# Kernel optimization log

Hardware: AMD Instinct MI355X
Metric: run time of the kernel (lower is better)

The kernel has to match this reference:

```python
import jax, jax.numpy as jnp
import numpy as np

NUM_HEADS = 8
NUM_LEVELS = 4
NUM_POINTS = 4
EMBED_DIM = 256
HEAD_DIM = EMBED_DIM // NUM_HEADS  # 32
SUM_POINTS = NUM_LEVELS * NUM_POINTS  # 16
OFFSET_SCALE = 0.5
SPATIAL = [(80, 80), (40, 40), (20, 20), (10, 10)]


def _bilinear_gather(v_flat, x, y, H, W):
    """grid_sample(bilinear, padding zeros, align_corners=False) via gathers.
    v_flat: (BN, c, H*W); x, y: (BN, Lq, P) pixel coords. -> (BN, c, Lq*P)"""
    BN = v_flat.shape[0]
    x0 = jnp.floor(x)
    y0 = jnp.floor(y)
    wx1 = x - x0
    wy1 = y - y0

    def corner(xi, yi, w):
        valid = (xi >= 0) & (xi <= W - 1) & (yi >= 0) & (yi <= H - 1)
        xc = jnp.clip(xi, 0, W - 1).astype(jnp.int32)
        yc = jnp.clip(yi, 0, H - 1).astype(jnp.int32)
        idx = (yc * W + xc).reshape(BN, -1)  # (BN, Lq*P)
        g = jnp.take_along_axis(v_flat, idx[:, None, :], axis=2)  # (BN, c, Lq*P)
        return g * (w * valid).reshape(BN, 1, -1)

    return (corner(x0, y0, (1.0 - wx1) * (1.0 - wy1))
            + corner(x0 + 1.0, y0, wx1 * (1.0 - wy1))
            + corner(x0, y0 + 1.0, (1.0 - wx1) * wy1)
            + corner(x0 + 1.0, y0 + 1.0, wx1 * wy1))


def setup_inputs() -> dict:
    key = jax.random.key(0)
    ks = jax.random.split(key, 6)
    bs, Lq = 16, 300
    spatial = np.array(SPATIAL, dtype=np.int64)
    Lv = int((spatial[:, 0] * spatial[:, 1]).sum())  # 8500

    query = jax.random.normal(ks[0], (bs, Lq, EMBED_DIM), jnp.float32)
    reference_points = jax.random.uniform(ks[1], (bs, Lq, 1, 4), jnp.float32)  # cx,cy,w,h in (0,1)
    value = jax.random.normal(ks[2], (bs, NUM_HEADS, HEAD_DIM, Lv), jnp.float32)

    W_off = jax.random.normal(ks[3], (EMBED_DIM, NUM_HEADS * SUM_POINTS * 2), jnp.float32) * 0.01
    # bias from _reset_parameters grid init
    thetas = np.arange(NUM_HEADS, dtype=np.float32) * (2.0 * np.pi / NUM_HEADS)
    grid = np.stack([np.cos(thetas), np.sin(thetas)], -1)
    grid = grid / np.abs(grid).max(-1, keepdims=True)
    grid = np.tile(grid.reshape(NUM_HEADS, 1, 2), (1, SUM_POINTS, 1))
    scaling = np.concatenate([np.arange(1, NUM_POINTS + 1) for _ in range(NUM_LEVELS)]).reshape(1, -1, 1)
    b_off = jnp.asarray((grid * scaling).reshape(-1), jnp.float32)

    W_attn = jax.random.normal(ks[4], (EMBED_DIM, NUM_HEADS * SUM_POINTS), jnp.float32) * 0.01
    b_attn = jnp.zeros((NUM_HEADS * SUM_POINTS,), jnp.float32)
    num_points_scale = jnp.full((SUM_POINTS,), 1.0 / NUM_POINTS, jnp.float32)

    return {"query": query, "reference_points": reference_points, "value": value,
            "value_spatial_shapes": spatial, "W_off": W_off, "b_off": b_off,
            "W_attn": W_attn, "b_attn": b_attn, "num_points_scale": num_points_scale}


def reference(query, reference_points, value, value_spatial_shapes,
              W_off, b_off, W_attn, b_attn, num_points_scale):
    bs, Lq, _ = query.shape
    BN = bs * NUM_HEADS

    off = (query @ W_off + b_off).reshape(bs, Lq, NUM_HEADS, SUM_POINTS, 2)
    attn = jax.nn.softmax((query @ W_attn + b_attn).reshape(bs, Lq, NUM_HEADS, SUM_POINTS), axis=-1)

    # box branch: reference_points (bs, Lq, 1, 4); [..., 2:] = wh scales offsets
    offset = off * num_points_scale[:, None] * reference_points[:, :, None, :, 2:] * OFFSET_SCALE
    loc = reference_points[:, :, None, :, :2] + offset  # (bs, Lq, H, SUM_POINTS, 2) in [0,1]

    grids = 2.0 * loc - 1.0
    grids = jnp.transpose(grids, (0, 2, 1, 3, 4)).reshape(BN, Lq, SUM_POINTS, 2)
    attn = jnp.transpose(attn, (0, 2, 1, 3)).reshape(BN, 1, Lq, SUM_POINTS)

    shapes = np.asarray(value_spatial_shapes)
    lvl_sizes = (shapes[:, 0] * shapes[:, 1]).tolist()
    v_levels = jnp.split(value.reshape(BN, HEAD_DIM, -1), np.cumsum(lvl_sizes)[:-1], axis=2)
    g_levels = jnp.split(grids, np.arange(NUM_POINTS, SUM_POINTS, NUM_POINTS), axis=2)

    sampled = []
    for (H, W), v_l, g_l in zip(shapes.tolist(), v_levels, g_levels):
        # align_corners=False pixel coords
        x = (g_l[..., 0] + 1.0) * (W * 0.5) - 0.5
        y = (g_l[..., 1] + 1.0) * (H * 0.5) - 0.5
        s = _bilinear_gather(v_l, x, y, H, W).reshape(BN, HEAD_DIM, Lq, NUM_POINTS)
        sampled.append(s)
    sampled = jnp.concatenate(sampled, axis=-1)  # (BN, c, Lq, SUM_POINTS)

    out = (sampled * attn).sum(-1)  # (BN, c, Lq)
    out = out.reshape(bs, NUM_HEADS * HEAD_DIM, Lq).transpose(0, 2, 1)  # (bs, Lq, embed_dim)
    return out
```

## Files before the change

kernel.cpp:

```cpp
#include <hip/hip_runtime.h>
#include <hip/hip_bf16.h>
#include <hip/hip_fp16.h>
#include <math.h>

#define BS 16
#define LQ 300
#define NH 8
#define HD 32
#define SP 16
#define ED 256
#define LV 8500
#define NB_BLK 300
#define PXT 256
#define TR_PER_BN 34
#define NTR_BLK (TR_PER_BN * 128)

static __device__ __forceinline__ int imin(int a, int b) { return a < b ? a : b; }
static __device__ __forceinline__ int imax(int a, int b) { return a > b ? a : b; }

static __device__ __forceinline__ unsigned f2bf(float x) {
    unsigned u = __float_as_uint(x);
    return (u + 0x7fffu + ((u >> 16) & 1u)) >> 16;
}

static __device__ __forceinline__ unsigned pk2h(float a, float b) {
    __half ha = __float2half_rn(a), hb = __float2half_rn(b);
    unsigned short ua = *reinterpret_cast<unsigned short*>(&ha);
    unsigned short ub = *reinterpret_cast<unsigned short*>(&hb);
    return (unsigned)ua | ((unsigned)ub << 16);
}

static __device__ __forceinline__ float2 up2h(unsigned u) {
    unsigned short ua = (unsigned short)(u & 0xffffu);
    unsigned short ub = (unsigned short)(u >> 16);
    __half ha = *reinterpret_cast<__half*>(&ua);
    __half hb = *reinterpret_cast<__half*>(&ub);
    return make_float2(__half2float(ha), __half2float(hb));
}

static __device__ __forceinline__ void gload16(const float* g, float* l) {
    __builtin_amdgcn_global_load_lds(
        (const __attribute__((address_space(1))) void*)g,
        (__attribute__((address_space(3))) void*)l, 16, 0, 0);
}

__global__ __launch_bounds__(256) void kF(const float* __restrict__ query,
                                          const float* __restrict__ refp,
                                          const float* __restrict__ Woff,
                                          const float* __restrict__ boff,
                                          const float* __restrict__ Wattn,
                                          const float* __restrict__ battn,
                                          const float* __restrict__ nps,
                                          unsigned* __restrict__ la,
                                          const float* __restrict__ v,
                                          __hip_bfloat16* __restrict__ vt,
                                          int nb) {
    __shared__ float s[32 * 256];
    const int tid = threadIdx.x;

    if ((int)blockIdx.x >= nb) {
        const int t   = blockIdx.x - nb;
        const int bn  = t / TR_PER_BN;
        const int px0 = (t - bn * TR_PER_BN) * PXT;
        const int nlv = imin(PXT, LV - px0);

        const int w = tid >> 6;
        const int l = tid & 63;
        if (l * 4 < nlv) {
            const float* src = v + ((size_t)bn * HD + w * 8) * LV + px0 + l * 4;
#pragma unroll
            for (int k = 0; k < 8; ++k)
                gload16(src + (size_t)k * LV, s + (w * 8 + k) * 256);
        }
        __syncthreads();
        const int p2 = tid >> 2;
        const int q  = tid & 3;
        char* dst0 = (char*)vt + ((size_t)bn * LV + px0) * (HD * 2) + q * 16;
#pragma unroll
        for (int j = 0; j < 4; ++j) {
            int p = p2 + 64 * j;
            if (p < nlv) {
                unsigned pk[4];
#pragma unroll
                for (int i = 0; i < 4; ++i) {
                    float f0 = s[(8 * q + 2 * i) * 256 + p];
                    float f1 = s[(8 * q + 2 * i + 1) * 256 + p];
                    pk[i] = f2bf(f0) | (f2bf(f1) << 16);
                }
                *reinterpret_cast<uint4*>(dst0 + (size_t)p * 64) =
                    make_uint4(pk[0], pk[1], pk[2], pk[3]);
            }
        }
        return;
    }

    float* qbuf = s;
    float* lbuf = s;
    const int gq0 = blockIdx.x * 16;

    const float* qsrc = query + (size_t)gq0 * ED;
#pragma unroll
    for (int i = 0; i < 16; ++i) qbuf[tid + 256 * i] = qsrc[tid + 256 * i];
    __syncthreads();

    const int qi = tid >> 5;
    const int cl = tid & 31;
    const float* qa = qbuf + qi * ED;
    const float* qb = qbuf + (qi + 8) * ED;

    float a0[4] = {0,0,0,0}, a1[4] = {0,0,0,0}, a2[4] = {0,0,0,0};
    float c0[4] = {0,0,0,0}, c1[4] = {0,0,0,0}, c2[4] = {0,0,0,0};
    const float4* w0 = (const float4*)(Woff + cl * 4);
    const float4* w1 = (const float4*)(Woff + 128 + cl * 4);
    const float4* w2 = (const float4*)(Wattn + cl * 4);
#pragma unroll 4
    for (int k = 0; k < ED; ++k) {
        float va = qa[k], vb = qb[k];
        float4 x0 = w0[k * 64];
        float4 x1 = w1[k * 64];
        float4 x2 = w2[k * 32];
        a0[0] += va * x0.x; a0[1] += va * x0.y; a0[2] += va * x0.z; a0[3] += va * x0.w;
        a1[0] += va * x1.x; a1[1] += va * x1.y; a1[2] += va * x1.z; a1[3] += va * x1.w;
        a2[0] += va * x2.x; a2[1] += va * x2.y; a2[2] += va * x2.z; a2[3] += va * x2.w;
        c0[0] += vb * x0.x; c0[1] += vb * x0.y; c0[2] += vb * x0.z; c0[3] += vb * x0.w;
        c1[0] += vb * x1.x; c1[1] += vb * x1.y; c1[2] += vb * x1.z; c1[3] += vb * x1.w;
        c2[0] += vb * x2.x; c2[1] += vb * x2.y; c2[2] += vb * x2.z; c2[3] += vb * x2.w;
    }
    __syncthreads();
    {
        float* ra = lbuf + qi * 384;
        float* rb = lbuf + (qi + 8) * 384;
#pragma unroll
        for (int u = 0; u < 4; ++u) {
            float bo0 = boff[cl * 4 + u];
            float bo1 = boff[128 + cl * 4 + u];
            float ba  = battn[cl * 4 + u];
            ra[cl * 4 + u]       = a0[u] + bo0;
            ra[128 + cl * 4 + u] = a1[u] + bo1;
            ra[256 + cl * 4 + u] = a2[u] + ba;
            rb[cl * 4 + u]       = c0[u] + bo0;
            rb[128 + cl * 4 + u] = c1[u] + bo1;
            rb[256 + cl * 4 + u] = c2[u] + ba;
        }
    }
    __syncthreads();

#pragma unroll
    for (int it = 0; it < 2; ++it) {
        const int slot = it * 256 + tid;
        const int qi2 = slot >> 5;
        const int h2  = (slot >> 2) & 7;
        const int pg  = slot & 3;
        const float* lr = lbuf + qi2 * 384;

        float l[4];
#pragma unroll
        for (int i = 0; i < 4; ++i) l[i] = lr[256 + h2 * 16 + pg * 4 + i];
        float m = fmaxf(fmaxf(l[0], l[1]), fmaxf(l[2], l[3]));
        m = fmaxf(m, __shfl_xor(m, 1));
        m = fmaxf(m, __shfl_xor(m, 2));
        float e[4];
        float ps = 0.f;
#pragma unroll
        for (int i = 0; i < 4; ++i) { e[i] = expf(l[i] - m); ps += e[i]; }
        ps += __shfl_xor(ps, 1);
        ps += __shfl_xor(ps, 2);
        float inv = 1.f / ps;

        const int gq = gq0 + qi2;
        const int b  = gq / LQ;
        const int q  = gq - b * LQ;
        const float* rp = refp + (size_t)gq * 4;
        float cx = rp[0], cy = rp[1], rw = rp[2], rh = rp[3];

        const int Wl = 80 >> pg;
        const int base = (25600 - (25600 >> (2 * pg))) / 3;
        const float fw = (float)Wl;

        unsigned* dst = la + ((((size_t)b * NH + h2) * LQ + q) * SP + pg * 4) * 4;
#pragma unroll
        for (int i = 0; i < 4; ++i) {
            int p = pg * 4 + i;
            float ox = lr[h2 * 32 + p * 2 + 0];
            float oy = lr[h2 * 32 + p * 2 + 1];
            float sc = nps[p] * 0.5f;
            float locx = cx + ox * sc * rw;
            float locy = cy + oy * sc * rh;
            float x = locx * fw - 0.5f;
            float y = locy * fw - 0.5f;
            float aw = e[i] * inv;

            float x0f = floorf(x), y0f = floorf(y);
            float fx = x - x0f, fy = y - y0f;
            int ix0 = (int)x0f, iy0 = (int)y0f;
            int ix1 = ix0 + 1, iy1 = iy0 + 1;
            bool vx0 = (ix0 >= 0) && (ix0 < Wl);
            bool vx1 = (ix1 >= 0) && (ix1 < Wl);
            bool vy0 = (iy0 >= 0) && (iy0 < Wl);
            bool vy1 = (iy1 >= 0) && (iy1 < Wl);
            int cx0 = imin(imax(ix0, 0), Wl - 1);
            int cx1 = imin(imax(ix1, 0), Wl - 1);
            int cy0 = imin(imax(iy0, 0), Wl - 1);
            int cy1 = imin(imax(iy1, 0), Wl - 1);
            float w00 = aw * (1.f - fx) * (1.f - fy) * ((vx0 && vy0) ? 1.f : 0.f);
            float w10 = aw * fx * (1.f - fy) * ((vx1 && vy0) ? 1.f : 0.f);
            float w01 = aw * (1.f - fx) * fy * ((vx0 && vy1) ? 1.f : 0.f);
            float w11 = aw * fx * fy * ((vx1 && vy1) ? 1.f : 0.f);
            unsigned i00 = (unsigned)(base + cy0 * Wl + cx0);
            unsigned i10 = (unsigned)(base + cy0 * Wl + cx1);
            unsigned i01 = (unsigned)(base + cy1 * Wl + cx0);
            unsigned i11 = (unsigned)(base + cy1 * Wl + cx1);

            *reinterpret_cast<uint4*>(dst + i * 4) =
                make_uint4(pk2h(w00, w10), pk2h(w01, w11),
                           i00 | (i10 << 16), i01 | (i11 << 16));
        }
    }
}

__global__ __launch_bounds__(128) void kC4(const __hip_bfloat16* __restrict__ vt,
                                           const unsigned* __restrict__ la,
                                           float* __restrict__ out) {
    const int bid = blockIdx.x;
    const int logical = (bid & 7) * 160 + (bid >> 3);
    const int bh = logical / 10;
    const int qt = logical - bh * 10;
    const int b = bh >> 3;
    const int h = bh & 7;

    const int tid = threadIdx.x;
    const int qs = tid >> 2;
    const int l4 = tid & 3;
    const int q = qt * 32 + qs;
    if (q >= LQ) return;

    const unsigned* lq = la + (((size_t)bh * LQ + q) * SP) * 4;
    const char* vb = (const char*)vt + (size_t)bh * LV * (HD * 2) + l4 * 16;

    float acc[8] = {0.f, 0.f, 0.f, 0.f, 0.f, 0.f, 0.f, 0.f};

#pragma unroll 2
    for (int p = 0; p < SP; p += 2) {
        uint4 rec0 = *reinterpret_cast<const uint4*>(lq + p * 4);
        uint4 rec1 = *reinterpret_cast<const uint4*>(lq + p * 4 + 4);
        uint4 r0 = *reinterpret_cast<const uint4*>(vb + (size_t)(rec0.z & 0xffffu) * 64);
        uint4 r1 = *reinterpret_cast<const uint4*>(vb + (size_t)(rec0.z >> 16) * 64);
        uint4 r2 = *reinterpret_cast<const uint4*>(vb + (size_t)(rec0.w & 0xffffu) * 64);
        uint4 r3 = *reinterpret_cast<const uint4*>(vb + (size_t)(rec0.w >> 16) * 64);
        uint4 r4 = *reinterpret_cast<const uint4*>(vb + (size_t)(rec1.z & 0xffffu) * 64);
        uint4 r5 = *reinterpret_cast<const uint4*>(vb + (size_t)(rec1.z >> 16) * 64);
        uint4 r6 = *reinterpret_cast<const uint4*>(vb + (size_t)(rec1.w & 0xffffu) * 64);
        uint4 r7 = *reinterpret_cast<const uint4*>(vb + (size_t)(rec1.w >> 16) * 64);
        float2 wA0 = up2h(rec0.x), wB0 = up2h(rec0.y);
        float2 wA1 = up2h(rec1.x), wB1 = up2h(rec1.y);
#define FMA8(W, R)                                                             \
        {                                                                      \
            union { unsigned u; float f; } _t;                                 \
            _t.u = (R).x << 16;         acc[0] = fmaf((W), _t.f, acc[0]);      \
            _t.u = (R).x & 0xffff0000u; acc[1] = fmaf((W), _t.f, acc[1]);      \
            _t.u = (R).y << 16;         acc[2] = fmaf((W), _t.f, acc[2]);      \
            _t.u = (R).y & 0xffff0000u; acc[3] = fmaf((W), _t.f, acc[3]);      \
            _t.u = (R).z << 16;         acc[4] = fmaf((W), _t.f, acc[4]);      \
            _t.u = (R).z & 0xffff0000u; acc[5] = fmaf((W), _t.f, acc[5]);      \
            _t.u = (R).w << 16;         acc[6] = fmaf((W), _t.f, acc[6]);      \
            _t.u = (R).w & 0xffff0000u; acc[7] = fmaf((W), _t.f, acc[7]);      \
        }
        FMA8(wA0.x, r0) FMA8(wA0.y, r1) FMA8(wB0.x, r2) FMA8(wB0.y, r3)
        FMA8(wA1.x, r4) FMA8(wA1.y, r5) FMA8(wB1.x, r6) FMA8(wB1.y, r7)
#undef FMA8
    }
    float* op = out + ((size_t)b * LQ + q) * ED + h * HD + l4 * 8;
    *reinterpret_cast<float4*>(op)     = make_float4(acc[0], acc[1], acc[2], acc[3]);
    *reinterpret_cast<float4*>(op + 4) = make_float4(acc[4], acc[5], acc[6], acc[7]);
}

__global__ __launch_bounds__(320) void kCfb(const float* __restrict__ val,
                                            const unsigned* __restrict__ la,
                                            float* __restrict__ out) {
    __shared__ __align__(16) unsigned sla[10 * SP * 4];
    int bid = blockIdx.x;
    int logical = (bid & 7) * 480 + (bid >> 3);
    int bh = logical / 30;
    int qt = logical - bh * 30;
    int b = bh >> 3;
    int h = bh & 7;
    const int tid = threadIdx.x;
    const unsigned* lsrc = la + (((size_t)bh * LQ + qt * 10) * SP) * 4;
    for (int i = tid; i < 640; i += 320) sla[i] = lsrc[i];
    __syncthreads();
    const int qs = tid >> 5;
    const int c  = tid & 31;
    const float* vb = val + ((size_t)bh * HD + c) * LV;
    float acc = 0.f;
    const unsigned* lq = sla + qs * (SP * 4);
#pragma unroll
    for (int p = 0; p < SP; ++p) {
        uint4 rec = *reinterpret_cast<const uint4*>(lq + p * 4);
        float2 wA = up2h(rec.x), wB = up2h(rec.y);
        acc += wA.x * vb[rec.z & 0xffffu];
        acc += wA.y * vb[rec.z >> 16];
        acc += wB.x * vb[rec.w & 0xffffu];
        acc += wB.y * vb[rec.w >> 16];
    }
    int q = qt * 10 + qs;
    out[((size_t)b * LQ + q) * ED + h * HD + c] = acc;
}

extern "C" void kernel_launch(void* const* d_in, const int* in_sizes, int n_in,
                              void* d_out, int out_size, void* d_ws, size_t ws_size,
                              hipStream_t stream) {
    const float* query = (const float*)d_in[0];
    const float* refp  = (const float*)d_in[1];
    const float* value = (const float*)d_in[2];
    const float* Woff  = (const float*)d_in[4];
    const float* boff  = (const float*)d_in[5];
    const float* Wattn = (const float*)d_in[6];
    const float* battn = (const float*)d_in[7];
    const float* nps   = (const float*)d_in[8];
    float* out = (float*)d_out;

    const size_t la_bytes = (size_t)BS * NH * LQ * SP * 16;
    const size_t vt_bytes = (size_t)BS * NH * LV * HD * sizeof(__hip_bfloat16);
    unsigned* la = (unsigned*)d_ws;
    __hip_bfloat16* vt = (__hip_bfloat16*)((char*)d_ws + la_bytes);
    const bool use_tr = ws_size >= la_bytes + vt_bytes;

    if (use_tr) {
        kF<<<dim3(NB_BLK + NTR_BLK), 256, 0, stream>>>(query, refp, Woff, boff,
                                                       Wattn, battn, nps, la,
                                                       value, vt, NB_BLK);
        kC4<<<dim3(1280), 128, 0, stream>>>(vt, la, out);
    } else {
        kF<<<dim3(NB_BLK), 256, 0, stream>>>(query, refp, Woff, boff,
                                             Wattn, battn, nps, la,
                                             value, (__hip_bfloat16*)nullptr, NB_BLK);
        kCfb<<<dim3(3840), 320, 0, stream>>>(value, la, out);
    }
}
```

Measured before the change: 72.57 us.

## Double-buffer value transpose tiles across multiple tiles per block

Each transpose block now handles 8 consecutive tiles instead of one. It double-buffers them in LDS, issuing the async global-to-LDS loads for the next tile while converting and storing the current one, with explicit vmcnt waits and barriers. The aim is to hide load latency and cut block launch overhead. It doubles the shared memory to 64KB per block, which lowers occupancy for both the transpose and projection paths and reduces the transpose grid to 544 blocks.

```diff
diff --git a/kernel.cpp b/kernel.cpp
--- a/kernel.cpp
+++ b/kernel.cpp
@@ -13,7 +13,9 @@
 #define NB_BLK 300
 #define PXT 256
 #define TR_PER_BN 34
-#define NTR_BLK (TR_PER_BN * 128)
+#define NTILES (TR_PER_BN * 128)
+#define TPB 8
+#define NTRB (NTILES / TPB)
 
 static __device__ __forceinline__ int imin(int a, int b) { return a < b ? a : b; }
 static __device__ __forceinline__ int imax(int a, int b) { return a > b ? a : b; }
@@ -55,47 +57,73 @@
                                           const float* __restrict__ v,
                                           __hip_bfloat16* __restrict__ vt,
                                           int nb) {
-    __shared__ float s[32 * 256];
+    __shared__ float s[2][32 * 256];
     const int tid = threadIdx.x;
 
     if ((int)blockIdx.x >= nb) {
-        const int t   = blockIdx.x - nb;
-        const int bn  = t / TR_PER_BN;
-        const int px0 = (t - bn * TR_PER_BN) * PXT;
-        const int nlv = imin(PXT, LV - px0);
-
-        const int w = tid >> 6;
-        const int l = tid & 63;
-        if (l * 4 < nlv) {
-            const float* src = v + ((size_t)bn * HD + w * 8) * LV + px0 + l * 4;
-#pragma unroll
-            for (int k = 0; k < 8; ++k)
-                gload16(src + (size_t)k * LV, s + (w * 8 + k) * 256);
-        }
-        __syncthreads();
-        const int p2 = tid >> 2;
-        const int q  = tid & 3;
-        char* dst0 = (char*)vt + ((size_t)bn * LV + px0) * (HD * 2) + q * 16;
-#pragma unroll
-        for (int j = 0; j < 4; ++j) {
-            int p = p2 + 64 * j;
-            if (p < nlv) {
-                unsigned pk[4];
-#pragma unroll
-                for (int i = 0; i < 4; ++i) {
-                    float f0 = s[(8 * q + 2 * i) * 256 + p];
-                    float f1 = s[(8 * q + 2 * i + 1) * 256 + p];
-                    pk[i] = f2bf(f0) | (f2bf(f1) << 16);
+        const int blk = blockIdx.x - nb;
+        const int t0  = blk * TPB;
+        const int w   = tid >> 6;
+        const int l   = tid & 63;
+        const int p2  = tid >> 2;
+        const int q   = tid & 3;
+
+        auto issue = [&](int t, float* buf) {
+            int bn  = t / TR_PER_BN;
+            int ti  = t - bn * TR_PER_BN;
+            int px0 = ti * PXT;
+            int nlv = imin(PXT, LV - px0);
+            if (l * 4 < nlv) {
+                const float* src = v + ((size_t)bn * HD + w * 8) * LV + px0 + l * 4;
+#pragma unroll
+                for (int k = 0; k < 8; ++k)
+                    gload16(src + (size_t)k * LV, buf + (w * 8 + k) * 256);
+            }
+        };
+
+        issue(t0, s[0]);
+
+#pragma unroll
+        for (int tt = 0; tt < TPB; ++tt) {
+            float* cur = s[tt & 1];
+            float* nxt = s[(tt & 1) ^ 1];
+            if (tt + 1 < TPB) {
+                issue(t0 + tt + 1, nxt);
+                asm volatile("s_waitcnt vmcnt(8)" ::: "memory");
+            } else {
+                asm volatile("s_waitcnt vmcnt(0)" ::: "memory");
+            }
+            __builtin_amdgcn_s_barrier();
+            __builtin_amdgcn_sched_barrier(0);
+
+            const int t  = t0 + tt;
+            const int bn = t / TR_PER_BN;
+            const int ti = t - bn * TR_PER_BN;
+            const int px0 = ti * PXT;
+            const int nlv = imin(PXT, LV - px0);
+            char* dst0 = (char*)vt + ((size_t)bn * LV + px0) * (HD * 2) + q * 16;
+#pragma unroll
+            for (int j = 0; j < 4; ++j) {
+                int p = p2 + 64 * j;
+                if (p < nlv) {
+                    unsigned pk[4];
+#pragma unroll
+                    for (int i = 0; i < 4; ++i) {
+                        float f0 = cur[(8 * q + 2 * i) * 256 + p];
+                        float f1 = cur[(8 * q + 2 * i + 1) * 256 + p];
+                        pk[i] = f2bf(f0) | (f2bf(f1) << 16);
+                    }
+                    *reinterpret_cast<uint4*>(dst0 + (size_t)p * 64) =
+                        make_uint4(pk[0], pk[1], pk[2], pk[3]);
                 }
-                *reinterpret_cast<uint4*>(dst0 + (size_t)p * 64) =
-                    make_uint4(pk[0], pk[1], pk[2], pk[3]);
             }
+            __builtin_amdgcn_s_barrier();
         }
         return;
     }
 
-    float* qbuf = s;
-    float* lbuf = s;
+    float* qbuf = s[0];
+    float* lbuf = s[0];
     const int gq0 = blockIdx.x * 16;
 
     const float* qsrc = query + (size_t)gq0 * ED;
@@ -326,9 +354,9 @@
     const bool use_tr = ws_size >= la_bytes + vt_bytes;
 
     if (use_tr) {
-        kF<<<dim3(NB_BLK + NTR_BLK), 256, 0, stream>>>(query, refp, Woff, boff,
-                                                       Wattn, battn, nps, la,
-                                                       value, vt, NB_BLK);
+        kF<<<dim3(NB_BLK + NTRB), 256, 0, stream>>>(query, refp, Woff, boff,
+                                                    Wattn, battn, nps, la,
+                                                    value, vt, NB_BLK);
         kC4<<<dim3(1280), 128, 0, stream>>>(vt, la, out);
     } else {
         kF<<<dim3(NB_BLK), 256, 0, stream>>>(query, refp, Woff, boff,
```

Result: faster. 70.21 us (median of 2 runs) (-3.3%).

## Transpose value to bf16 with direct register loads over fewer, larger chunks

Applied to the files above, without the earlier changes.

The value-transpose blocks no longer stage data through LDS with async global_load_lds. Each wave now loads 8 channels per pixel straight into registers, packs them to bf16 and writes 16-byte stores, looping over a 1088-pixel chunk per block. This uses 8 blocks per batch-head instead of 34 and shrinks shared memory. The aim is to drop LDS traffic and the barrier and to cut block count, at the cost of strided 4-byte global reads and less parallelism per block.

```diff
diff --git a/kernel.cpp b/kernel.cpp
--- a/kernel.cpp
+++ b/kernel.cpp
@@ -11,9 +11,9 @@
 #define ED 256
 #define LV 8500
 #define NB_BLK 300
-#define PXT 256
-#define TR_PER_BN 34
-#define NTR_BLK (TR_PER_BN * 128)
+#define CHUNKS 8
+#define CHPX 1088
+#define NTR_BLK (128 * CHUNKS)
 
 static __device__ __forceinline__ int imin(int a, int b) { return a < b ? a : b; }
 static __device__ __forceinline__ int imax(int a, int b) { return a > b ? a : b; }
@@ -36,12 +36,6 @@
     __half ha = *reinterpret_cast<__half*>(&ua);
     __half hb = *reinterpret_cast<__half*>(&ub);
     return make_float2(__half2float(ha), __half2float(hb));
-}
-
-static __device__ __forceinline__ void gload16(const float* g, float* l) {
-    __builtin_amdgcn_global_load_lds(
-        (const __attribute__((address_space(1))) void*)g,
-        (__attribute__((address_space(3))) void*)l, 16, 0, 0);
 }
 
 __global__ __launch_bounds__(256) void kF(const float* __restrict__ query,
@@ -55,41 +49,32 @@
                                           const float* __restrict__ v,
                                           __hip_bfloat16* __restrict__ vt,
                                           int nb) {
-    __shared__ float s[32 * 256];
+    __shared__ float s[16 * 384];
     const int tid = threadIdx.x;
 
     if ((int)blockIdx.x >= nb) {
-        const int t   = blockIdx.x - nb;
-        const int bn  = t / TR_PER_BN;
-        const int px0 = (t - bn * TR_PER_BN) * PXT;
-        const int nlv = imin(PXT, LV - px0);
-
-        const int w = tid >> 6;
-        const int l = tid & 63;
-        if (l * 4 < nlv) {
-            const float* src = v + ((size_t)bn * HD + w * 8) * LV + px0 + l * 4;
-#pragma unroll
-            for (int k = 0; k < 8; ++k)
-                gload16(src + (size_t)k * LV, s + (w * 8 + k) * 256);
-        }
-        __syncthreads();
-        const int p2 = tid >> 2;
-        const int q  = tid & 3;
-        char* dst0 = (char*)vt + ((size_t)bn * LV + px0) * (HD * 2) + q * 16;
-#pragma unroll
-        for (int j = 0; j < 4; ++j) {
-            int p = p2 + 64 * j;
-            if (p < nlv) {
-                unsigned pk[4];
-#pragma unroll
-                for (int i = 0; i < 4; ++i) {
-                    float f0 = s[(8 * q + 2 * i) * 256 + p];
-                    float f1 = s[(8 * q + 2 * i + 1) * 256 + p];
-                    pk[i] = f2bf(f0) | (f2bf(f1) << 16);
-                }
-                *reinterpret_cast<uint4*>(dst0 + (size_t)p * 64) =
-                    make_uint4(pk[0], pk[1], pk[2], pk[3]);
-            }
+        const int t     = blockIdx.x - nb;
+        const int bn    = t >> 3;
+        const int chunk = t & 7;
+        const int px0   = chunk * CHPX;
+        const int pxe   = imin(px0 + CHPX, LV);
+        const int w     = tid >> 6;
+        const int l     = tid & 63;
+
+        const float* src = v + ((size_t)bn * HD + w * 8) * LV;
+        char* dst = (char*)vt + (size_t)bn * LV * (HD * 2) + w * 16;
+
+#pragma unroll 2
+        for (int p = px0 + l; p < pxe; p += 64) {
+            float r[8];
+#pragma unroll
+            for (int k = 0; k < 8; ++k) r[k] = src[(size_t)k * LV + p];
+            unsigned pk[4];
+#pragma unroll
+            for (int k = 0; k < 4; ++k)
+                pk[k] = f2bf(r[2 * k]) | (f2bf(r[2 * k + 1]) << 16);
+            *reinterpret_cast<uint4*>(dst + (size_t)p * 64) =
+                make_uint4(pk[0], pk[1], pk[2], pk[3]);
         }
         return;
     }
```

Measured after the change: 126.2 us. +73.9%, slower.
